# Kernel tuning notes

Measured on AMD Instinct MI355X. Metric: run time of the kernel, lower is better.

The kernel has to match this reference:

```python
import jax, jax.numpy as jnp
import numpy as np

F0 = 39          # FIELD_COUNT
D = 16           # embedding dim
SIZES = [128, 128, 128]  # cross_layer_sizes
B = 8192


def setup_inputs() -> dict:
    key = jax.random.key(0)
    k0, k1, k2, k3, k4 = jax.random.split(key, 5)
    nn_input = jax.random.normal(k0, (B, F0 * D), dtype=jnp.float32)
    # direct=False => field_nums: [39, 64, 64]; filters: [F0*Fk, L]
    scale = 0.02
    f0 = jax.random.normal(k1, (F0 * F0, SIZES[0]), dtype=jnp.float32) * scale
    f1 = jax.random.normal(k2, (F0 * (SIZES[0] // 2), SIZES[1]), dtype=jnp.float32) * scale
    f2 = jax.random.normal(k3, (F0 * (SIZES[1] // 2), SIZES[2]), dtype=jnp.float32) * scale
    final_len = SIZES[0] // 2 + SIZES[1] // 2 + SIZES[2]  # 256
    w_nn = jax.random.normal(k4, (final_len, 1), dtype=jnp.float32) * scale
    b_nn = jnp.zeros((1,), dtype=jnp.float32)
    return {"nn_input": nn_input, "f0": f0, "f1": f1, "f2": f2,
            "w_nn": w_nn, "b_nn": b_nn}


def reference(nn_input, f0, f1, f2, w_nn, b_nn):
    x0 = nn_input.reshape(-1, F0, D)            # [B, F0, D]
    b = x0.shape[0]
    filters = [f0, f1, f2]
    hidden = x0
    field = F0
    direct_outs = []
    n_layers = len(SIZES)
    for idx, layer_size in enumerate(SIZES):
        # dim-wise outer product: z[b,d,i*field+j] = x0[b,i,d]*hidden[b,j,d]
        z = jnp.einsum('bid,bjd->bdij', x0, hidden).reshape(b, D, F0 * field)
        if idx == 0:
            # remove self-interactions: keep strictly upper triangle, x2
            mask = jnp.triu(jnp.ones((F0, F0), dtype=z.dtype), k=1).reshape(1, 1, F0 * F0)
            z = z * mask * 2.0
        # conv1d kernel-width-1 == per-position GEMM; fuse the [0,2,1] transpose
        curr = jnp.einsum('bdc,cl->bld', z, filters[idx])   # [B, L, D]
        curr = jax.nn.relu(curr)                            # cross_activation='relu'
        if idx != n_layers - 1:
            half = layer_size // 2
            next_hidden = curr[:, :half, :]
            direct = curr[:, half:, :]
        else:
            direct = curr
            next_hidden = None
        direct_outs.append(direct)
        hidden = next_hidden
        field = layer_size // 2
    result = jnp.concatenate(direct_outs, axis=1)   # [B, final_len, D]
    rs = result.sum(axis=-1)                        # [B, final_len]
    base_score = rs.sum(axis=1, keepdims=True)      # res=True
    return base_score + rs @ w_nn + b_nn            # [B, 1]
```

## Files before the change

### kernel.cpp

```cpp
#include <hip/hip_runtime.h>


#define F0N 39
#define NB  32
#define NC16 156
#define LAYER_HALVES (NC16 * 4 * 64 * 8)

typedef _Float16 half8 __attribute__((ext_vector_type(8)));
typedef float f32x16 __attribute__((ext_vector_type(16)));

__global__ void prep_kernel(const float* __restrict__ f0,
                            const float* __restrict__ f1,
                            const float* __restrict__ f2,
                            _Float16* __restrict__ fprep) {
    int blk  = blockIdx.x;
    int l    = blk / NC16;
    int c16  = blk - l * NC16;
    int t    = threadIdx.x;
    int nt   = t >> 6;
    int lane = t & 63;
    int hf   = lane >> 5;
    int n    = nt * 32 + (lane & 31);
    const float* f = (l == 0) ? f0 : ((l == 1) ? f1 : f2);
    half8 v;
    #pragma unroll
    for (int reg = 0; reg < 8; ++reg) {
        int kg = c16 * 16 + hf * 8 + reg;
        float x;
        if (l == 0) {
            int fi = kg >> 6, fj = kg & 63;
            x = (fj < F0N && fj > fi) ? 2.0f * f[(fi * F0N + fj) * 128 + n] : 0.0f;
        } else {
            x = f[(size_t)kg * 128 + n];
        }
        v[reg] = (_Float16)x;
    }
    *(half8*)&fprep[(size_t)l * LAYER_HALVES + (((c16 * 4 + nt) * 64 + lane) << 3)] = v;
}

#define FULL_STEP(Q)                                                          \
    do {                                                                      \
        const _Float16* bq = fpl + ((((size_t)(i * 4 + (Q)) * 4 + nh2) * 64 + lane) << 3); \
        half8 Bf0 = *(const half8*)bq;                                        \
        half8 Bf1 = *(const half8*)(bq + 512);                                \
        _Pragma("unroll")                                                     \
        for (int mt = 0; mt < 4; ++mt) {                                      \
            half8 hA = *(const half8*)&hT[abase[mt] + (Q) * 16];              \
            half8 Af = hA * xv2[mt];                                          \
            acc[mt][0] = __builtin_amdgcn_mfma_f32_32x32x16_f16(              \
                Af, Bf0, acc[mt][0], 0, 0, 0);                                \
            acc[mt][1] = __builtin_amdgcn_mfma_f32_32x32x16_f16(              \
                Af, Bf1, acc[mt][1], 0, 0, 0);                                \
        }                                                                     \
    } while (0)

__global__ __launch_bounds__(512, 2) void cin_mfma(
    const float* __restrict__ xin,
    const _Float16* __restrict__ fprep,
    const float* __restrict__ wnn,
    const float* __restrict__ bnn,
    float* __restrict__ out)
{
    __shared__ _Float16 hT[NB * 16 * 72] __attribute__((aligned(16)));
    __shared__ _Float16 xs[NB * 16 * 40] __attribute__((aligned(16)));
    __shared__ float outacc[NB];

    const int t     = threadIdx.x;
    const int wave  = t >> 6;
    const int lane  = t & 63;
    const int hf    = lane >> 5;
    const int lane5 = lane & 31;
    const int dl    = lane & 15;
    const int bt    = lane5 >> 4;
    const int bg    = wave >> 1;
    const int nh2   = (wave & 1) * 2;
    const int b0    = blockIdx.x * NB;

    for (int u = t; u < NB * 16 * 72 / 8; u += 512) ((uint4*)hT)[u] = uint4{0, 0, 0, 0};
    if (t < NB) outacc[t] = 0.0f;
    __syncthreads();

    for (int u = t; u < NB * F0N; u += 512) {
        int nb = u / F0N;
        int i  = u - nb * F0N;
        const float* src = xin + (size_t)(b0 + nb) * 624 + i * 16;
        #pragma unroll
        for (int q = 0; q < 4; ++q) {
            float4 v = *(const float4*)(src + q * 4);
            int d = q * 4;
            hT[(nb * 16 + d + 0) * 72 + i] = (_Float16)v.x;
            hT[(nb * 16 + d + 1) * 72 + i] = (_Float16)v.y;
            hT[(nb * 16 + d + 2) * 72 + i] = (_Float16)v.z;
            hT[(nb * 16 + d + 3) * 72 + i] = (_Float16)v.w;
            xs[(nb * 16 + d + 0) * 40 + i] = (_Float16)v.x;
            xs[(nb * 16 + d + 1) * 40 + i] = (_Float16)v.y;
            xs[(nb * 16 + d + 2) * 40 + i] = (_Float16)v.z;
            xs[(nb * 16 + d + 3) * 40 + i] = (_Float16)v.w;
        }
    }
    __syncthreads();

    int abase[4], xrow[4];
    #pragma unroll
    for (int mt = 0; mt < 4; ++mt) {
        abase[mt] = ((bg * 8 + mt * 2 + bt) * 16 + dl) * 72 + hf * 8;
        xrow[mt]  = ((bg * 8 + mt * 2 + bt) * 16 + dl) * 40;
    }

    for (int layer = 0; layer < 3; ++layer) {
        f32x16 acc[4][2];
        #pragma unroll
        for (int mt = 0; mt < 4; ++mt)
            #pragma unroll
            for (int nt = 0; nt < 2; ++nt)
                #pragma unroll
                for (int e = 0; e < 16; ++e) acc[mt][nt][e] = 0.0f;

        const _Float16* fpl = fprep + (size_t)layer * LAYER_HALVES;

        if (layer == 0) {
            _Float16 xv2[4];
            for (int i = 0; i < 16; ++i) {
                #pragma unroll
                for (int mt = 0; mt < 4; ++mt) xv2[mt] = xs[xrow[mt] + i];
                if (i < 15) FULL_STEP(0);
                FULL_STEP(1);
                FULL_STEP(2);
            }
            for (int i = 16; i < 32; ++i) {
                #pragma unroll
                for (int mt = 0; mt < 4; ++mt) xv2[mt] = xs[xrow[mt] + i];
                if (i < 31) FULL_STEP(1);
                FULL_STEP(2);
            }
            for (int i = 32; i < 38; ++i) {
                #pragma unroll
                for (int mt = 0; mt < 4; ++mt) xv2[mt] = xs[xrow[mt] + i];
                FULL_STEP(2);
            }
        } else {
            _Float16 xv2[4];
            for (int i = 0; i < F0N; ++i) {
                #pragma unroll
                for (int mt = 0; mt < 4; ++mt) xv2[mt] = xs[xrow[mt] + i];
                FULL_STEP(0);
                FULL_STEP(1);
                FULL_STEP(2);
                FULL_STEP(3);
            }
        }

        __syncthreads();

        const int catbase = (layer == 2) ? 128 : ((layer == 0) ? -64 : 0);
        #pragma unroll
        for (int mt = 0; mt < 4; ++mt) {
            const int nb0 = bg * 8 + mt * 2;
            float cm0 = 0.0f, cm1 = 0.0f;
            #pragma unroll
            for (int nt = 0; nt < 2; ++nt) {
                const int gnt = nh2 + nt;
                float r[16];
                #pragma unroll
                for (int reg = 0; reg < 16; ++reg)
                    r[reg] = fmaxf(acc[mt][nt][reg], 0.0f);
                if (layer < 2 && gnt < 2) {
                    const int j = gnt * 32 + lane5;
                    #pragma unroll
                    for (int reg = 0; reg < 16; ++reg) {
                        int nb = nb0 + (reg >> 3);
                        int d  = (reg & 3) + 8 * ((reg >> 2) & 1) + 4 * hf;
                        hT[(nb * 16 + d) * 72 + j] = (_Float16)r[reg];
                    }
                }
                if (layer == 2 || gnt >= 2) {
                    const float w = 1.0f + wnn[catbase + gnt * 32 + lane5];
                    float s0 = ((r[0] + r[1]) + (r[2] + r[3])) +
                               ((r[4] + r[5]) + (r[6] + r[7]));
                    float s1 = ((r[8] + r[9]) + (r[10] + r[11])) +
                               ((r[12] + r[13]) + (r[14] + r[15]));
                    s0 += __shfl_xor(s0, 32, 64);
                    s1 += __shfl_xor(s1, 32, 64);
                    cm0 = fmaf(s0, w, cm0);
                    cm1 = fmaf(s1, w, cm1);
                }
            }
            #pragma unroll
            for (int sh = 16; sh >= 1; sh >>= 1) {
                cm0 += __shfl_xor(cm0, sh, 64);
                cm1 += __shfl_xor(cm1, sh, 64);
            }
            if (lane == 0 && (nh2 == 2 || layer == 2)) {
                atomicAdd(&outacc[nb0], cm0);
                atomicAdd(&outacc[nb0 + 1], cm1);
            }
        }
        __syncthreads();
    }

    if (t < NB) out[b0 + t] = outacc[t] + bnn[0];
}

extern "C" void kernel_launch(void* const* d_in, const int* in_sizes, int n_in,
                              void* d_out, int out_size, void* d_ws, size_t ws_size,
                              hipStream_t stream) {
    const float* xin = (const float*)d_in[0];
    const float* f0g = (const float*)d_in[1];
    const float* f1g = (const float*)d_in[2];
    const float* f2g = (const float*)d_in[3];
    const float* wnn = (const float*)d_in[4];
    const float* bnn = (const float*)d_in[5];
    float* out = (float*)d_out;
    _Float16* fprep = (_Float16*)d_ws;

    prep_kernel<<<3 * NC16, 256, 0, stream>>>(f0g, f1g, f2g, fprep);

    const int B = in_sizes[0] / 624;
    cin_mfma<<<B / NB, 512, 0, stream>>>(xin, fprep, wnn, bnn, out);
}
```

Before: 285.4 us.

## Shrink batch tile to 8 rows and hold hidden A-fragments in registers

```diff
diff --git a/kernel.cpp b/kernel.cpp
--- a/kernel.cpp
+++ b/kernel.cpp
@@ -2,7 +2,7 @@
 
 
 #define F0N 39
-#define NB  32
+#define NB  8
 #define NC16 156
 #define LAYER_HALVES (NC16 * 4 * 64 * 8)
 
@@ -43,18 +43,15 @@
         const _Float16* bq = fpl + ((((size_t)(i * 4 + (Q)) * 4 + nh2) * 64 + lane) << 3); \
         half8 Bf0 = *(const half8*)bq;                                        \
         half8 Bf1 = *(const half8*)(bq + 512);                                \
-        _Pragma("unroll")                                                     \
-        for (int mt = 0; mt < 4; ++mt) {                                      \
-            half8 hA = *(const half8*)&hT[abase[mt] + (Q) * 16];              \
-            half8 Af = hA * xv2[mt];                                          \
-            acc[mt][0] = __builtin_amdgcn_mfma_f32_32x32x16_f16(              \
-                Af, Bf0, acc[mt][0], 0, 0, 0);                                \
-            acc[mt][1] = __builtin_amdgcn_mfma_f32_32x32x16_f16(              \
-                Af, Bf1, acc[mt][1], 0, 0, 0);                                \
-        }                                                                     \
+        half8 Af0 = hreg[0][(Q)] * xv2[0];                                    \
+        half8 Af1 = hreg[1][(Q)] * xv2[1];                                    \
+        acc[0][0] = __builtin_amdgcn_mfma_f32_32x32x16_f16(Af0, Bf0, acc[0][0], 0, 0, 0); \
+        acc[0][1] = __builtin_amdgcn_mfma_f32_32x32x16_f16(Af0, Bf1, acc[0][1], 0, 0, 0); \
+        acc[1][0] = __builtin_amdgcn_mfma_f32_32x32x16_f16(Af1, Bf0, acc[1][0], 0, 0, 0); \
+        acc[1][1] = __builtin_amdgcn_mfma_f32_32x32x16_f16(Af1, Bf1, acc[1][1], 0, 0, 0); \
     } while (0)
 
-__global__ __launch_bounds__(512, 2) void cin_mfma(
+__global__ __launch_bounds__(256, 3) void cin_mfma(
     const float* __restrict__ xin,
     const _Float16* __restrict__ fprep,
     const float* __restrict__ wnn,
@@ -72,15 +69,15 @@
     const int lane5 = lane & 31;
     const int dl    = lane & 15;
     const int bt    = lane5 >> 4;
-    const int bg    = wave >> 1;
+    const int mp4   = (wave >> 1) * 4;
     const int nh2   = (wave & 1) * 2;
     const int b0    = blockIdx.x * NB;
 
-    for (int u = t; u < NB * 16 * 72 / 8; u += 512) ((uint4*)hT)[u] = uint4{0, 0, 0, 0};
+    for (int u = t; u < NB * 16 * 72 / 8; u += 256) ((uint4*)hT)[u] = uint4{0, 0, 0, 0};
     if (t < NB) outacc[t] = 0.0f;
     __syncthreads();
 
-    for (int u = t; u < NB * F0N; u += 512) {
+    for (int u = t; u < NB * F0N; u += 256) {
         int nb = u / F0N;
         int i  = u - nb * F0N;
         const float* src = xin + (size_t)(b0 + nb) * 624 + i * 16;
@@ -100,49 +97,54 @@
     }
     __syncthreads();
 
-    int abase[4], xrow[4];
-    #pragma unroll
-    for (int mt = 0; mt < 4; ++mt) {
-        abase[mt] = ((bg * 8 + mt * 2 + bt) * 16 + dl) * 72 + hf * 8;
-        xrow[mt]  = ((bg * 8 + mt * 2 + bt) * 16 + dl) * 40;
-    }
-
     for (int layer = 0; layer < 3; ++layer) {
-        f32x16 acc[4][2];
-        #pragma unroll
-        for (int mt = 0; mt < 4; ++mt)
+        half8 hreg[2][4];
+        #pragma unroll
+        for (int mt = 0; mt < 2; ++mt) {
+            int base = ((mp4 + mt * 2 + bt) * 16 + dl) * 72 + hf * 8;
+            #pragma unroll
+            for (int r = 0; r < 4; ++r)
+                hreg[mt][r] = *(const half8*)&hT[base + r * 16];
+        }
+        __syncthreads();
+
+        f32x16 acc[2][2];
+        #pragma unroll
+        for (int mt = 0; mt < 2; ++mt)
             #pragma unroll
             for (int nt = 0; nt < 2; ++nt)
                 #pragma unroll
                 for (int e = 0; e < 16; ++e) acc[mt][nt][e] = 0.0f;
 
         const _Float16* fpl = fprep + (size_t)layer * LAYER_HALVES;
+        const int xrow0 = ((mp4 + bt) * 16 + dl) * 40;
+        const int xrow1 = ((mp4 + 2 + bt) * 16 + dl) * 40;
 
         if (layer == 0) {
-            _Float16 xv2[4];
+            _Float16 xv2[2];
             for (int i = 0; i < 16; ++i) {
-                #pragma unroll
-                for (int mt = 0; mt < 4; ++mt) xv2[mt] = xs[xrow[mt] + i];
+                xv2[0] = xs[xrow0 + i];
+                xv2[1] = xs[xrow1 + i];
                 if (i < 15) FULL_STEP(0);
                 FULL_STEP(1);
                 FULL_STEP(2);
             }
             for (int i = 16; i < 32; ++i) {
-                #pragma unroll
-                for (int mt = 0; mt < 4; ++mt) xv2[mt] = xs[xrow[mt] + i];
+                xv2[0] = xs[xrow0 + i];
+                xv2[1] = xs[xrow1 + i];
                 if (i < 31) FULL_STEP(1);
                 FULL_STEP(2);
             }
             for (int i = 32; i < 38; ++i) {
-                #pragma unroll
-                for (int mt = 0; mt < 4; ++mt) xv2[mt] = xs[xrow[mt] + i];
+                xv2[0] = xs[xrow0 + i];
+                xv2[1] = xs[xrow1 + i];
                 FULL_STEP(2);
             }
         } else {
-            _Float16 xv2[4];
+            _Float16 xv2[2];
             for (int i = 0; i < F0N; ++i) {
-                #pragma unroll
-                for (int mt = 0; mt < 4; ++mt) xv2[mt] = xs[xrow[mt] + i];
+                xv2[0] = xs[xrow0 + i];
+                xv2[1] = xs[xrow1 + i];
                 FULL_STEP(0);
                 FULL_STEP(1);
                 FULL_STEP(2);
@@ -150,12 +152,10 @@
             }
         }
 
-        __syncthreads();
-
         const int catbase = (layer == 2) ? 128 : ((layer == 0) ? -64 : 0);
         #pragma unroll
-        for (int mt = 0; mt < 4; ++mt) {
-            const int nb0 = bg * 8 + mt * 2;
+        for (int mt = 0; mt < 2; ++mt) {
+            const int nb0 = mp4 + mt * 2;
             float cm0 = 0.0f, cm1 = 0.0f;
             #pragma unroll
             for (int nt = 0; nt < 2; ++nt) {
@@ -216,5 +216,5 @@
     prep_kernel<<<3 * NC16, 256, 0, stream>>>(f0g, f1g, f2g, fprep);
 
     const int B = in_sizes[0] / 624;
-    cin_mfma<<<B / NB, 512, 0, stream>>>(xin, fprep, wnn, bnn, out);
+    cin_mfma<<<B / NB, 256, 0, stream>>>(xin, fprep, wnn, bnn, out);
 }
```

Measured after the change: 324.9 us. +13.8%, slower.
